# Kernel tuning notes

Hardware: AMD Instinct MI355X
Metric: run time of the kernel (lower is better)

Reference implementation:

```python
import jax, jax.numpy as jnp
import numpy as np
import math

B, T, C = 1, 2048, 2048
H, KVH = 32, 8
D = C // H  # 64
EPS = 1e-5
ROPE_THETA = 10000.0


def rmsnorm(x, w):
    # RMSNorm over last axis (head_dim), matches flax RMSNorm applied per-head
    var = jnp.mean(jnp.square(x), axis=-1, keepdims=True)
    return x * jax.lax.rsqrt(var + EPS) * w


def apply_rope(x, cos, sin):
    # x: [B, T, h, D]; cos/sin: [T, D//2]
    xr = x.reshape(*x.shape[:-1], D // 2, 2)
    x0, x1 = xr[..., 0], xr[..., 1]
    c = cos.reshape(1, T, 1, D // 2)
    s = sin.reshape(1, T, 1, D // 2)
    o0 = x0 * c - x1 * s
    o1 = x0 * s + x1 * c
    return jnp.stack([o0, o1], axis=-1).reshape(x.shape)


def setup_inputs() -> dict:
    key = jax.random.key(0)
    ks = jax.random.split(key, 12)
    x = jax.random.normal(ks[0], (B, T, C), jnp.float32)
    # RoPE tables
    inv_freq = 1.0 / (ROPE_THETA ** (np.arange(0, D, 2, dtype=np.float32) / D))
    angles = np.arange(T, dtype=np.float32)[:, None] * inv_freq[None, :]  # [T, D//2]
    freqs_cos = jnp.asarray(np.cos(angles))
    freqs_sin = jnp.asarray(np.sin(angles))
    # causal additive mask [1,1,T,T]
    causal = np.triu(np.full((T, T), -1e9, dtype=np.float32), k=1)
    mask = jnp.asarray(causal)[None, None]
    sc = lambda f: 1.0 / math.sqrt(f)
    return {
        "x": x,
        "freqs_cos": freqs_cos,
        "freqs_sin": freqs_sin,
        "mask": mask,
        "wq_k": jax.random.normal(ks[1], (C, H * D), jnp.float32) * sc(C),
        "wq_b": jnp.zeros((H * D,), jnp.float32),
        "wk_k": jax.random.normal(ks[2], (C, KVH * D), jnp.float32) * sc(C),
        "wk_b": jnp.zeros((KVH * D,), jnp.float32),
        "wv_k": jax.random.normal(ks[3], (C, KVH * D), jnp.float32) * sc(C),
        "wv_b": jnp.zeros((KVH * D,), jnp.float32),
        "wo_k": jax.random.normal(ks[4], (H * D, C), jnp.float32) * sc(H * D),
        "wo_b": jnp.zeros((C,), jnp.float32),
        "qn_w": jnp.ones((D,), jnp.float32),
        "kn_w": jnp.ones((D,), jnp.float32),
    }


def reference(x, freqs_cos, freqs_sin, mask, wq_k, wq_b, wk_k, wk_b, wv_k, wv_b, wo_k, wo_b, qn_w, kn_w):
    q = (x @ wq_k + wq_b).reshape(B, T, H, D)
    k = (x @ wk_k + wk_b).reshape(B, T, KVH, D)
    v = (x @ wv_k + wv_b).reshape(B, T, KVH, D)
    # QK RMSNorm over head_dim
    q = rmsnorm(q, qn_w)
    k = rmsnorm(k, kn_w)
    # RoPE
    q = apply_rope(q, freqs_cos, freqs_sin)
    k = apply_rope(k, freqs_cos, freqs_sin)
    # GQA repeat kv heads
    rep = H // KVH
    k = jnp.repeat(k, rep, axis=2)
    v = jnp.repeat(v, rep, axis=2)
    # [B, H, T, D]
    q, k, v = (jnp.swapaxes(t, 1, 2) for t in (q, k, v))
    scale = 1.0 / math.sqrt(D)
    scores = jnp.einsum("bhqd,bhkd->bhqk", q, k) * scale + mask
    attn = jax.nn.softmax(scores, axis=-1)
    out = jnp.einsum("bhqk,bhkd->bhqd", attn, v)
    out = jnp.swapaxes(out, 1, 2).reshape(B, T, H * D)
    return out @ wo_k + wo_b
```

## Files before the change

### kernel.cpp

```cpp
#include <hip/hip_runtime.h>
#include <hip/hip_bf16.h>
#include <cstdint>

typedef unsigned short u16;
typedef __attribute__((ext_vector_type(8))) short short8;
typedef __attribute__((ext_vector_type(4))) float f32x4;

__device__ __forceinline__ u16 f2bf(float f) {
  union { float f; uint32_t u; } c; c.f = f;
  return (u16)((c.u + 0x7FFFu + ((c.u >> 16) & 1u)) >> 16);
}

__device__ __forceinline__ uint32_t pack_bf16x2(float a, float b) {
  union { __hip_bfloat162 h; uint32_t u; } c;
  c.h = __float22bfloat162_rn(make_float2(a, b));
  return c.u;
}

__global__ __launch_bounds__(256) void prep_kernel(const float* __restrict__ x,
                                                   u16* __restrict__ xb,
                                                   const float* __restrict__ wq,
                                                   const float* __restrict__ wk,
                                                   const float* __restrict__ wv,
                                                   const float* __restrict__ wo,
                                                   u16* __restrict__ wqkvT,
                                                   u16* __restrict__ woT) {
  int id = blockIdx.x;
  if (id >= 2560) {
    int i = (id - 2560) * 256 + threadIdx.x;
    float4 v = ((const float4*)x)[i];
    ((ushort4*)xb)[i] = make_ushort4(f2bf(v.x), f2bf(v.y), f2bf(v.z), f2bf(v.w));
    return;
  }
  __shared__ float tile[64][65];
  const int K = 2048;
  int bx = id % 80, by = id / 80;
  const float* in; u16* out; int N, nx;
  if (bx < 32)      { in = wq; out = wqkvT;                          N = 2048; nx = bx; }
  else if (bx < 40) { in = wk; out = wqkvT + (size_t)2048 * 2048;    N = 512;  nx = bx - 32; }
  else if (bx < 48) { in = wv; out = wqkvT + (size_t)2560 * 2048;    N = 512;  nx = bx - 40; }
  else              { in = wo; out = woT;                            N = 2048; nx = bx - 48; }
  int n0 = nx * 64, k0 = by * 64;
  int t = threadIdx.x;
  int a = t & 63, b4 = t >> 6;
#pragma unroll
  for (int j = 0; j < 16; ++j) {
    int kk = j * 4 + b4;
    tile[kk][a] = in[(size_t)(k0 + kk) * N + n0 + a];
  }
  __syncthreads();
#pragma unroll
  for (int j = 0; j < 16; ++j) {
    int nn = j * 4 + b4;
    out[(size_t)(n0 + nn) * K + k0 + a] = f2bf(tile[a][nn]);
  }
}

__global__ __launch_bounds__(256, 3) void gemm_qkv(const u16* __restrict__ A,
                                                   const u16* __restrict__ Bt,
                                                   const float* __restrict__ wq_b,
                                                   const float* __restrict__ wk_b,
                                                   const float* __restrict__ wv_b,
                                                   const float* __restrict__ qn_w,
                                                   const float* __restrict__ kn_w,
                                                   const float* __restrict__ fc,
                                                   const float* __restrict__ fs,
                                                   u16* __restrict__ Qg,
                                                   u16* __restrict__ Kg,
                                                   u16* __restrict__ Vgt) {
  const int K = 2048, nb = 24;
  __shared__ alignas(16) u16 As[2][64 * 64];
  __shared__ alignas(16) u16 Bs[2][128 * 64];
  int nwg = gridDim.x;
  int cpx = nwg >> 3;
  int bid = blockIdx.x;
  int swz = (bid & 7) * cpx + (bid >> 3);
  int m0 = (swz / nb) << 6;
  int n0 = (swz % nb) << 7;
  int tid = threadIdx.x;
  int w = tid >> 6, lane = tid & 63;
  int wr = w >> 1, wc = w & 1;
  int fr = lane & 15, hi = lane >> 4;
  int sw = fr & 7;

  auto STAGE = [&](int buf, int kt) {
#pragma unroll
    for (int i = 0; i < 2; ++i) {
      int chunk = i * 256 + tid;
      int row = chunk >> 3, c = chunk & 7;
      const u16* ga = A + (size_t)(m0 + row) * K + kt + ((c ^ (row & 7)) << 3);
      u16* la = &As[buf][(size_t)(i * 256 + w * 64) * 8];
      __builtin_amdgcn_global_load_lds((const __attribute__((address_space(1))) void*)ga,
                                       (__attribute__((address_space(3))) void*)la, 16, 0, 0);
    }
#pragma unroll
    for (int i = 0; i < 4; ++i) {
      int chunk = i * 256 + tid;
      int row = chunk >> 3, c = chunk & 7;
      const u16* gb = Bt + (size_t)(n0 + row) * K + kt + ((c ^ (row & 7)) << 3);
      u16* lb = &Bs[buf][(size_t)(i * 256 + w * 64) * 8];
      __builtin_amdgcn_global_load_lds((const __attribute__((address_space(1))) void*)gb,
                                       (__attribute__((address_space(3))) void*)lb, 16, 0, 0);
    }
  };

  f32x4 acc[2][4] = {};
  STAGE(0, 0);
  __syncthreads();
  int cur = 0;
  int c0 = (hi ^ sw) << 3, c1 = ((4 + hi) ^ sw) << 3;
  for (int kt = 0; kt < K; kt += 64) {
    if (kt + 64 < K) STAGE(cur ^ 1, kt + 64);
    short8 af[2][2], bf[4][2];
#pragma unroll
    for (int m = 0; m < 2; ++m) {
      int rb = (wr * 32 + m * 16 + fr) * 64;
      af[m][0] = *(const short8*)&As[cur][rb + c0];
      af[m][1] = *(const short8*)&As[cur][rb + c1];
    }
#pragma unroll
    for (int n = 0; n < 4; ++n) {
      int rb = (wc * 64 + n * 16 + fr) * 64;
      bf[n][0] = *(const short8*)&Bs[cur][rb + c0];
      bf[n][1] = *(const short8*)&Bs[cur][rb + c1];
    }
#pragma unroll
    for (int m = 0; m < 2; ++m)
#pragma unroll
      for (int n = 0; n < 4; ++n) {
        acc[m][n] = __builtin_amdgcn_mfma_f32_16x16x32_bf16(af[m][0], bf[n][0], acc[m][n], 0, 0, 0);
        acc[m][n] = __builtin_amdgcn_mfma_f32_16x16x32_bf16(af[m][1], bf[n][1], acc[m][n], 0, 0, 0);
      }
    __syncthreads();
    cur ^= 1;
  }

  int fbase = n0 + wc * 64;
  if (fbase >= 2560) {
    const float* bias = wv_b + (fbase - 2560);
    u16* vt = Vgt + (size_t)(fbase - 2560) * 2048;
    float bv[4];
#pragma unroll
    for (int n = 0; n < 4; ++n) bv[n] = bias[n * 16 + fr];
#pragma unroll
    for (int m = 0; m < 2; ++m)
#pragma unroll
      for (int r = 0; r < 4; ++r) {
        int t = m0 + wr * 32 + m * 16 + hi * 4 + r;
#pragma unroll
        for (int n = 0; n < 4; ++n)
          vt[(size_t)(n * 16 + fr) * 2048 + t] = f2bf(acc[m][n][r] + bv[n]);
      }
    return;
  }
  bool isQ = (fbase < 2048);
  const float* bias = isQ ? wq_b + fbase : wk_b + (fbase - 2048);
  const float* nw   = isQ ? qn_w : kn_w;
  float nscale      = isQ ? 0.18033688f : 1.0f;
  u16* outp = isQ ? Qg + (size_t)(fbase >> 6) * 2048 * 64
                  : Kg + (size_t)((fbase - 2048) >> 6) * 2048 * 64;
  float bv[4], nwv[4];
#pragma unroll
  for (int n = 0; n < 4; ++n) {
    bv[n] = bias[n * 16 + fr];
    nwv[n] = nw[n * 16 + fr] * nscale;
  }
#pragma unroll
  for (int m = 0; m < 2; ++m) {
#pragma unroll
    for (int r = 0; r < 4; ++r) {
      int t = m0 + wr * 32 + m * 16 + hi * 4 + r;
      float v[4];
      float sq = 0.0f;
#pragma unroll
      for (int n = 0; n < 4; ++n) { v[n] = acc[m][n][r] + bv[n]; sq += v[n] * v[n]; }
      sq += __shfl_xor(sq, 1); sq += __shfl_xor(sq, 2);
      sq += __shfl_xor(sq, 4); sq += __shfl_xor(sq, 8);
      float rr = rsqrtf(sq * (1.0f / 64.0f) + 1e-5f);
#pragma unroll
      for (int n = 0; n < 4; ++n) {
        float vn = v[n] * rr * nwv[n];
        float part = __shfl_xor(vn, 1);
        int dh = n * 16 + fr;
        float c = fc[t * 32 + (dh >> 1)];
        float s = fs[t * 32 + (dh >> 1)];
        v[n] = (dh & 1) ? (part * s + vn * c) : (vn * c - part * s);
      }
#pragma unroll
      for (int n = 0; n < 4; ++n)
        outp[(size_t)t * 64 + n * 16 + fr] = f2bf(v[n]);
    }
  }
}

__global__ __launch_bounds__(256, 3) void gemm_bt(const u16* __restrict__ A,
                                                  const u16* __restrict__ Bt,
                                                  float* __restrict__ C,
                                                  const float* __restrict__ bias,
                                                  int M, int N, int K) {
  __shared__ alignas(16) u16 As[2][64 * 64];
  __shared__ alignas(16) u16 Bs[2][128 * 64];
  int nb = N >> 7;
  int nwg = gridDim.x;
  int cpx = nwg >> 3;
  int bid = blockIdx.x;
  int swz = (bid & 7) * cpx + (bid >> 3);
  int m0 = (swz / nb) << 6;
  int n0 = (swz % nb) << 7;
  int tid = threadIdx.x;
  int w = tid >> 6, lane = tid & 63;
  int wr = w >> 1, wc = w & 1;
  int fr = lane & 15, hi = lane >> 4;
  int sw = fr & 7;

  auto STAGE = [&](int buf, int kt) {
#pragma unroll
    for (int i = 0; i < 2; ++i) {
      int chunk = i * 256 + tid;
      int row = chunk >> 3, c = chunk & 7;
      const u16* ga = A + (size_t)(m0 + row) * K + kt + ((c ^ (row & 7)) << 3);
      u16* la = &As[buf][(size_t)(i * 256 + w * 64) * 8];
      __builtin_amdgcn_global_load_lds((const __attribute__((address_space(1))) void*)ga,
                                       (__attribute__((address_space(3))) void*)la, 16, 0, 0);
    }
#pragma unroll
    for (int i = 0; i < 4; ++i) {
      int chunk = i * 256 + tid;
      int row = chunk >> 3, c = chunk & 7;
      const u16* gb = Bt + (size_t)(n0 + row) * K + kt + ((c ^ (row & 7)) << 3);
      u16* lb = &Bs[buf][(size_t)(i * 256 + w * 64) * 8];
      __builtin_amdgcn_global_load_lds((const __attribute__((address_space(1))) void*)gb,
                                       (__attribute__((address_space(3))) void*)lb, 16, 0, 0);
    }
  };

  f32x4 acc[2][4] = {};
  STAGE(0, 0);
  __syncthreads();
  int cur = 0;
  int c0 = (hi ^ sw) << 3, c1 = ((4 + hi) ^ sw) << 3;
  for (int kt = 0; kt < K; kt += 64) {
    if (kt + 64 < K) STAGE(cur ^ 1, kt + 64);
    short8 af[2][2], bf[4][2];
#pragma unroll
    for (int m = 0; m < 2; ++m) {
      int rb = (wr * 32 + m * 16 + fr) * 64;
      af[m][0] = *(const short8*)&As[cur][rb + c0];
      af[m][1] = *(const short8*)&As[cur][rb + c1];
    }
#pragma unroll
    for (int n = 0; n < 4; ++n) {
      int rb = (wc * 64 + n * 16 + fr) * 64;
      bf[n][0] = *(const short8*)&Bs[cur][rb + c0];
      bf[n][1] = *(const short8*)&Bs[cur][rb + c1];
    }
#pragma unroll
    for (int m = 0; m < 2; ++m)
#pragma unroll
      for (int n = 0; n < 4; ++n) {
        acc[m][n] = __builtin_amdgcn_mfma_f32_16x16x32_bf16(af[m][0], bf[n][0], acc[m][n], 0, 0, 0);
        acc[m][n] = __builtin_amdgcn_mfma_f32_16x16x32_bf16(af[m][1], bf[n][1], acc[m][n], 0, 0, 0);
      }
    __syncthreads();
    cur ^= 1;
  }
#pragma unroll
  for (int m = 0; m < 2; ++m) {
#pragma unroll
    for (int n = 0; n < 4; ++n) {
      int gcol = n0 + wc * 64 + n * 16 + fr;
      float bvx = bias ? bias[gcol] : 0.0f;
#pragma unroll
      for (int r = 0; r < 4; ++r) {
        int grow = m0 + wr * 32 + m * 16 + hi * 4 + r;
        C[(size_t)grow * N + gcol] = acc[m][n][r] + bvx;
      }
    }
  }
}

__global__ __launch_bounds__(256, 3) void attn_kernel(const u16* __restrict__ Qg,
                                                      const u16* __restrict__ Kg,
                                                      const u16* __restrict__ Vgt,
                                                      const float* __restrict__ qn_w,
                                                      const float* __restrict__ kn_w,
                                                      u16* __restrict__ att) {
  __shared__ alignas(16) u16 Ks[2][64 * 64];
  __shared__ alignas(16) u16 Vs[2][64 * 64];
  __shared__ alignas(16) uint32_t Ps[4][16 * 36];

  int bid = blockIdx.x;
  int grp = bid >> 8, idx = bid & 255;
  int q0 = idx >> 5, h = idx & 31;
  int qt = (grp == 0) ? q0 : (grp == 1) ? 15 - q0 : (grp == 2) ? 16 + q0 : 31 - q0;
  int kvh = h >> 2;

  int tid = threadIdx.x, w = tid >> 6, lane = tid & 63;
  int fr = lane & 15, hi = lane >> 4, fk = hi * 8;

  float ba = fabsf(qn_w[lane]), bb = fabsf(kn_w[lane]);
#pragma unroll
  for (int off = 32; off >= 1; off >>= 1) {
    ba = fmaxf(ba, __shfl_xor(ba, off));
    bb = fmaxf(bb, __shfl_xor(bb, off));
  }
  float mfix = 11.5416222f * ba * bb;

  const u16* qbase = Qg + ((size_t)h * 2048 + qt * 64 + w * 16 + fr) * 64;
  short8 qf0 = *(const short8*)(qbase + fk);
  short8 qf1 = *(const short8*)(qbase + 32 + fk);
  f32x4 o[4] = {};
  float lrow = 0.0f;

  const u16* Kbase = Kg + (size_t)kvh * 2048 * 64;
  const u16* Vtbase = Vgt + (size_t)kvh * 64 * 2048;
  int row0 = tid >> 3, cc = tid & 7;

  auto stage = [&](int buf, int kt) {
#pragma unroll
    for (int i = 0; i < 2; ++i) {
      int row = i * 32 + row0;
      const u16* srcK = Kbase + ((size_t)(kt * 64 + row)) * 64 + ((cc ^ (row & 7)) << 3);
      u16* dstK = &Ks[buf][(size_t)(i * 256 + w * 64) * 8];
      __builtin_amdgcn_global_load_lds((const __attribute__((address_space(1))) void*)srcK,
                                       (__attribute__((address_space(3))) void*)dstK, 16, 0, 0);
      const u16* srcV = Vtbase + (size_t)row * 2048 + kt * 64 + ((cc ^ (row & 7)) << 3);
      u16* dstV = &Vs[buf][(size_t)(i * 256 + w * 64) * 8];
      __builtin_amdgcn_global_load_lds((const __attribute__((address_space(1))) void*)srcV,
                                       (__attribute__((address_space(3))) void*)dstV, 16, 0, 0);
    }
  };

  stage(0, 0);
  __syncthreads();

  uint32_t* Pw = &Ps[w][0];
  int swzr = (fr & 7) << 4;
  int qrow = qt * 64 + w * 16 + fr;

  for (int kt = 0; kt <= qt; ++kt) {
    int buf = kt & 1;
    bool diag = (kt == qt);
    if (!diag) stage(buf ^ 1, kt + 1);
    const char* KsB = (const char*)&Ks[buf][0];
    const char* VsB = (const char*)&Vs[buf][0];
    f32x4 s4[4] = {};
    __builtin_amdgcn_s_setprio(1);
#pragma unroll
    for (int g = 0; g < 4; ++g) {
      int rb = (g * 16 + fr) * 128;
      short8 b0 = *(const short8*)(KsB + ((rb + hi * 16) ^ swzr));
      short8 b1 = *(const short8*)(KsB + ((rb + 64 + hi * 16) ^ swzr));
      s4[g] = __builtin_amdgcn_mfma_f32_16x16x32_bf16(b0, qf0, s4[g], 0, 0, 0);
      s4[g] = __builtin_amdgcn_mfma_f32_16x16x32_bf16(b1, qf1, s4[g], 0, 0, 0);
    }
    __builtin_amdgcn_s_setprio(0);
    if (diag) {
      int kbase = kt * 64 + hi * 4;
#pragma unroll
      for (int g = 0; g < 4; ++g)
#pragma unroll
        for (int r = 0; r < 4; ++r)
          if (kbase + g * 16 + r > qrow) s4[g][r] = -1e30f;
    }
#pragma unroll
    for (int g = 0; g < 4; ++g) {
      float p0 = exp2f(s4[g][0] - mfix);
      float p1 = exp2f(s4[g][1] - mfix);
      float p2 = exp2f(s4[g][2] - mfix);
      float p3 = exp2f(s4[g][3] - mfix);
      lrow += (p0 + p1) + (p2 + p3);
      uint2 pk = make_uint2(pack_bf16x2(p0, p1), pack_bf16x2(p2, p3));
      *(uint2*)&Pw[fr * 36 + g * 8 + hi * 2] = pk;
    }
    asm volatile("s_waitcnt lgkmcnt(0)" ::: "memory");
    short8 pa0 = *(const short8*)&Pw[fr * 36 + hi * 4];
    short8 pa1 = *(const short8*)&Pw[fr * 36 + 16 + hi * 4];
    __builtin_amdgcn_s_setprio(1);
#pragma unroll
    for (int g2 = 0; g2 < 4; ++g2) {
      int rb = (g2 * 16 + fr) * 128;
      short8 vb0 = *(const short8*)(VsB + ((rb + hi * 16) ^ swzr));
      short8 vb1 = *(const short8*)(VsB + ((rb + 64 + hi * 16) ^ swzr));
      o[g2] = __builtin_amdgcn_mfma_f32_16x16x32_bf16(pa0, vb0, o[g2], 0, 0, 0);
      o[g2] = __builtin_amdgcn_mfma_f32_16x16x32_bf16(pa1, vb1, o[g2], 0, 0, 0);
    }
    __builtin_amdgcn_s_setprio(0);
    __syncthreads();
  }
  float rtot = lrow;
  rtot += __shfl_xor(rtot, 16);
  rtot += __shfl_xor(rtot, 32);
#pragma unroll
  for (int r = 0; r < 4; ++r) {
    float li = __shfl(rtot, hi * 4 + r);
    float inv = 1.0f / li;
    size_t rowoff = (size_t)(qt * 64 + w * 16 + hi * 4 + r) * 2048 + h * 64;
#pragma unroll
    for (int g2 = 0; g2 < 4; ++g2)
      att[rowoff + g2 * 16 + fr] = f2bf(o[g2][r] * inv);
  }
}

extern "C" void kernel_launch(void* const* d_in, const int* in_sizes, int n_in,
                              void* d_out, int out_size, void* d_ws, size_t ws_size,
                              hipStream_t stream) {
  const float* x    = (const float*)d_in[0];
  const float* fc   = (const float*)d_in[1];
  const float* fs   = (const float*)d_in[2];
  const float* wq   = (const float*)d_in[4];
  const float* wq_b = (const float*)d_in[5];
  const float* wk   = (const float*)d_in[6];
  const float* wk_b = (const float*)d_in[7];
  const float* wv   = (const float*)d_in[8];
  const float* wv_b = (const float*)d_in[9];
  const float* wo   = (const float*)d_in[10];
  const float* wo_b = (const float*)d_in[11];
  const float* qn   = (const float*)d_in[12];
  const float* kn   = (const float*)d_in[13];
  float* out = (float*)d_out;

  char* ws = (char*)d_ws;
  u16*  xb    = (u16*)(ws);
  u16*  wqkvT = (u16*)(ws + (size_t)(8  << 20));
  u16*  woT   = (u16*)(ws + (size_t)(20 << 20));
  u16*  Qg    = (u16*)(ws + (size_t)(52 << 20));
  u16*  Kg    = (u16*)(ws + (size_t)(60 << 20));
  u16*  Vgt   = (u16*)(ws + (size_t)(62 << 20));
  u16*  att   = (u16*)(ws + (size_t)(64 << 20));

  prep_kernel<<<6656, 256, 0, stream>>>(x, xb, wq, wk, wv, wo, wqkvT, woT);
  gemm_qkv<<<32 * 24, 256, 0, stream>>>(xb, wqkvT, wq_b, wk_b, wv_b, qn, kn, fc, fs, Qg, Kg, Vgt);
  attn_kernel<<<1024, 256, 0, stream>>>(Qg, Kg, Vgt, qn, kn, att);
  gemm_bt<<<32 * 16, 256, 0, stream>>>(att, woT, out, wo_b, 2048, 2048, 2048);
}
```

Before: 134.0 us.

## Process two adjacent query tiles per attention block to reuse K/V tiles

Each attention block now handles two consecutive 64-row query tiles (2p and 2p+1), so each K/V tile staged in shared memory is used for both. This halves the grid to 512 blocks and roughly halves K/V global traffic and staging overhead. Staging changes from direct global-to-LDS loads to register-staged loads written after compute, and launch bounds drop to 2 waves per SIMD for the extra registers. The risks are lower occupancy, fewer blocks to balance the causal triangle, and less latency hiding.

```diff
diff --git a/kernel.cpp b/kernel.cpp
--- a/kernel.cpp
+++ b/kernel.cpp
@@ -279,7 +279,7 @@
   }
 }
 
-__global__ __launch_bounds__(256, 3) void attn_kernel(const u16* __restrict__ Qg,
+__global__ __launch_bounds__(256, 2) void attn_kernel(const u16* __restrict__ Qg,
                                                       const u16* __restrict__ Kg,
                                                       const u16* __restrict__ Vgt,
                                                       const float* __restrict__ qn_w,
@@ -287,12 +287,13 @@
                                                       u16* __restrict__ att) {
   __shared__ alignas(16) u16 Ks[2][64 * 64];
   __shared__ alignas(16) u16 Vs[2][64 * 64];
-  __shared__ alignas(16) uint32_t Ps[4][16 * 36];
+  __shared__ alignas(16) uint32_t Ps[2][4][16 * 36];
 
   int bid = blockIdx.x;
   int grp = bid >> 8, idx = bid & 255;
   int q0 = idx >> 5, h = idx & 31;
-  int qt = (grp == 0) ? q0 : (grp == 1) ? 15 - q0 : (grp == 2) ? 16 + q0 : 31 - q0;
+  int p = (grp == 0) ? q0 : 15 - q0;
+  int qa = 2 * p, qb = 2 * p + 1;
   int kvh = h >> 2;
 
   int tid = threadIdx.x, w = tid >> 6, lane = tid & 63;
@@ -306,99 +307,167 @@
   }
   float mfix = 11.5416222f * ba * bb;
 
-  const u16* qbase = Qg + ((size_t)h * 2048 + qt * 64 + w * 16 + fr) * 64;
-  short8 qf0 = *(const short8*)(qbase + fk);
-  short8 qf1 = *(const short8*)(qbase + 32 + fk);
-  f32x4 o[4] = {};
-  float lrow = 0.0f;
-
+  const u16* qbaseA = Qg + ((size_t)h * 2048 + qa * 64 + w * 16 + fr) * 64;
+  const u16* qbaseB = Qg + ((size_t)h * 2048 + qb * 64 + w * 16 + fr) * 64;
+  short8 qfa0 = *(const short8*)(qbaseA + fk);
+  short8 qfa1 = *(const short8*)(qbaseA + 32 + fk);
+  short8 qfb0 = *(const short8*)(qbaseB + fk);
+  short8 qfb1 = *(const short8*)(qbaseB + 32 + fk);
+  f32x4 oa[4] = {}, ob[4] = {};
+  float lrowa = 0.0f, lrowb = 0.0f;
+
+  int row0 = tid >> 3, cc = tid & 7;
   const u16* Kbase = Kg + (size_t)kvh * 2048 * 64;
   const u16* Vtbase = Vgt + (size_t)kvh * 64 * 2048;
-  int row0 = tid >> 3, cc = tid & 7;
-
-  auto stage = [&](int buf, int kt) {
-#pragma unroll
-    for (int i = 0; i < 2; ++i) {
-      int row = i * 32 + row0;
-      const u16* srcK = Kbase + ((size_t)(kt * 64 + row)) * 64 + ((cc ^ (row & 7)) << 3);
-      u16* dstK = &Ks[buf][(size_t)(i * 256 + w * 64) * 8];
-      __builtin_amdgcn_global_load_lds((const __attribute__((address_space(1))) void*)srcK,
-                                       (__attribute__((address_space(3))) void*)dstK, 16, 0, 0);
-      const u16* srcV = Vtbase + (size_t)row * 2048 + kt * 64 + ((cc ^ (row & 7)) << 3);
-      u16* dstV = &Vs[buf][(size_t)(i * 256 + w * 64) * 8];
-      __builtin_amdgcn_global_load_lds((const __attribute__((address_space(1))) void*)srcV,
-                                       (__attribute__((address_space(3))) void*)dstV, 16, 0, 0);
-    }
+
+  short8 k0r, k1r, v0r, v1r;
+  auto stage_load = [&](int kt2) {
+    const u16* kb = Kbase + (size_t)kt2 * 64 * 64;
+    k0r = *(const short8*)(kb + row0 * 64 + cc * 8);
+    k1r = *(const short8*)(kb + (32 + row0) * 64 + cc * 8);
+    const u16* vb = Vtbase + (size_t)row0 * 2048 + kt2 * 64 + cc * 8;
+    v0r = *(const short8*)vb;
+    v1r = *(const short8*)(vb + 32 * 2048);
   };
-
-  stage(0, 0);
+  auto stage_write = [&](int buf) {
+    char* KsB = (char*)&Ks[buf][0];
+    char* VsB = (char*)&Vs[buf][0];
+    int offA = (row0 * 128 + cc * 16) ^ ((row0 & 7) << 4);
+    int offB = ((32 + row0) * 128 + cc * 16) ^ ((row0 & 7) << 4);
+    *(short8*)(KsB + offA) = k0r;
+    *(short8*)(KsB + offB) = k1r;
+    *(short8*)(VsB + offA) = v0r;
+    *(short8*)(VsB + offB) = v1r;
+  };
+
+  stage_load(0);
+  stage_write(0);
   __syncthreads();
 
-  uint32_t* Pw = &Ps[w][0];
   int swzr = (fr & 7) << 4;
-  int qrow = qt * 64 + w * 16 + fr;
-
-  for (int kt = 0; kt <= qt; ++kt) {
+  int qrowA = qa * 64 + w * 16 + fr;
+  int qrowB = qb * 64 + w * 16 + fr;
+  int nkt = qb + 1;
+
+  for (int kt = 0; kt < nkt; ++kt) {
     int buf = kt & 1;
-    bool diag = (kt == qt);
-    if (!diag) stage(buf ^ 1, kt + 1);
+    bool lastIter = (kt == qb);
+    if (!lastIter) stage_load(kt + 1);
     const char* KsB = (const char*)&Ks[buf][0];
     const char* VsB = (const char*)&Vs[buf][0];
-    f32x4 s4[4] = {};
-    __builtin_amdgcn_s_setprio(1);
-#pragma unroll
-    for (int g = 0; g < 4; ++g) {
-      int rb = (g * 16 + fr) * 128;
-      short8 b0 = *(const short8*)(KsB + ((rb + hi * 16) ^ swzr));
-      short8 b1 = *(const short8*)(KsB + ((rb + 64 + hi * 16) ^ swzr));
-      s4[g] = __builtin_amdgcn_mfma_f32_16x16x32_bf16(b0, qf0, s4[g], 0, 0, 0);
-      s4[g] = __builtin_amdgcn_mfma_f32_16x16x32_bf16(b1, qf1, s4[g], 0, 0, 0);
-    }
-    __builtin_amdgcn_s_setprio(0);
-    if (diag) {
-      int kbase = kt * 64 + hi * 4;
-#pragma unroll
-      for (int g = 0; g < 4; ++g)
-#pragma unroll
-        for (int r = 0; r < 4; ++r)
-          if (kbase + g * 16 + r > qrow) s4[g][r] = -1e30f;
-    }
-#pragma unroll
-    for (int g = 0; g < 4; ++g) {
-      float p0 = exp2f(s4[g][0] - mfix);
-      float p1 = exp2f(s4[g][1] - mfix);
-      float p2 = exp2f(s4[g][2] - mfix);
-      float p3 = exp2f(s4[g][3] - mfix);
-      lrow += (p0 + p1) + (p2 + p3);
-      uint2 pk = make_uint2(pack_bf16x2(p0, p1), pack_bf16x2(p2, p3));
-      *(uint2*)&Pw[fr * 36 + g * 8 + hi * 2] = pk;
-    }
-    asm volatile("s_waitcnt lgkmcnt(0)" ::: "memory");
-    short8 pa0 = *(const short8*)&Pw[fr * 36 + hi * 4];
-    short8 pa1 = *(const short8*)&Pw[fr * 36 + 16 + hi * 4];
-    __builtin_amdgcn_s_setprio(1);
+
+    if (kt <= qa) {
+      f32x4 s4[4] = {};
+      __builtin_amdgcn_s_setprio(1);
+#pragma unroll
+      for (int g = 0; g < 4; ++g) {
+        int rb = (g * 16 + fr) * 128;
+        short8 b0 = *(const short8*)(KsB + ((rb + hi * 16) ^ swzr));
+        short8 b1 = *(const short8*)(KsB + ((rb + 64 + hi * 16) ^ swzr));
+        s4[g] = __builtin_amdgcn_mfma_f32_16x16x32_bf16(b0, qfa0, s4[g], 0, 0, 0);
+        s4[g] = __builtin_amdgcn_mfma_f32_16x16x32_bf16(b1, qfa1, s4[g], 0, 0, 0);
+      }
+      __builtin_amdgcn_s_setprio(0);
+      if (kt == qa) {
+        int kbase = kt * 64 + hi * 4;
+#pragma unroll
+        for (int g = 0; g < 4; ++g)
+#pragma unroll
+          for (int r = 0; r < 4; ++r)
+            if (kbase + g * 16 + r > qrowA) s4[g][r] = -1e30f;
+      }
+      uint32_t* Pw = &Ps[0][w][0];
+#pragma unroll
+      for (int g = 0; g < 4; ++g) {
+        float p0 = exp2f(s4[g][0] - mfix);
+        float p1 = exp2f(s4[g][1] - mfix);
+        float p2 = exp2f(s4[g][2] - mfix);
+        float p3 = exp2f(s4[g][3] - mfix);
+        lrowa += (p0 + p1) + (p2 + p3);
+        uint2 pk = make_uint2(pack_bf16x2(p0, p1), pack_bf16x2(p2, p3));
+        *(uint2*)&Pw[fr * 36 + g * 8 + hi * 2] = pk;
+      }
+      asm volatile("s_waitcnt lgkmcnt(0)" ::: "memory");
+      short8 pa0 = *(const short8*)&Pw[fr * 36 + hi * 4];
+      short8 pa1 = *(const short8*)&Pw[fr * 36 + 16 + hi * 4];
+      __builtin_amdgcn_s_setprio(1);
+#pragma unroll
+      for (int g2 = 0; g2 < 4; ++g2) {
+        int rb = (g2 * 16 + fr) * 128;
+        short8 vb0 = *(const short8*)(VsB + ((rb + hi * 16) ^ swzr));
+        short8 vb1 = *(const short8*)(VsB + ((rb + 64 + hi * 16) ^ swzr));
+        oa[g2] = __builtin_amdgcn_mfma_f32_16x16x32_bf16(pa0, vb0, oa[g2], 0, 0, 0);
+        oa[g2] = __builtin_amdgcn_mfma_f32_16x16x32_bf16(pa1, vb1, oa[g2], 0, 0, 0);
+      }
+      __builtin_amdgcn_s_setprio(0);
+    }
+
+    {
+      f32x4 s4[4] = {};
+      __builtin_amdgcn_s_setprio(1);
+#pragma unroll
+      for (int g = 0; g < 4; ++g) {
+        int rb = (g * 16 + fr) * 128;
+        short8 b0 = *(const short8*)(KsB + ((rb + hi * 16) ^ swzr));
+        short8 b1 = *(const short8*)(KsB + ((rb + 64 + hi * 16) ^ swzr));
+        s4[g] = __builtin_amdgcn_mfma_f32_16x16x32_bf16(b0, qfb0, s4[g], 0, 0, 0);
+        s4[g] = __builtin_amdgcn_mfma_f32_16x16x32_bf16(b1, qfb1, s4[g], 0, 0, 0);
+      }
+      __builtin_amdgcn_s_setprio(0);
+      if (lastIter) {
+        int kbase = kt * 64 + hi * 4;
+#pragma unroll
+        for (int g = 0; g < 4; ++g)
+#pragma unroll
+          for (int r = 0; r < 4; ++r)
+            if (kbase + g * 16 + r > qrowB) s4[g][r] = -1e30f;
+      }
+      uint32_t* Pw = &Ps[1][w][0];
+#pragma unroll
+      for (int g = 0; g < 4; ++g) {
+        float p0 = exp2f(s4[g][0] - mfix);
+        float p1 = exp2f(s4[g][1] - mfix);
+        float p2 = exp2f(s4[g][2] - mfix);
+        float p3 = exp2f(s4[g][3] - mfix);
+        lrowb += (p0 + p1) + (p2 + p3);
+        uint2 pk = make_uint2(pack_bf16x2(p0, p1), pack_bf16x2(p2, p3));
+        *(uint2*)&Pw[fr * 36 + g * 8 + hi * 2] = pk;
+      }
+      asm volatile("s_waitcnt lgkmcnt(0)" ::: "memory");
+      short8 pa0 = *(const short8*)&Pw[fr * 36 + hi * 4];
+      short8 pa1 = *(const short8*)&Pw[fr * 36 + 16 + hi * 4];
+      __builtin_amdgcn_s_setprio(1);
+#pragma unroll
+      for (int g2 = 0; g2 < 4; ++g2) {
+        int rb = (g2 * 16 + fr) * 128;
+        short8 vb0 = *(const short8*)(VsB + ((rb + hi * 16) ^ swzr));
+        short8 vb1 = *(const short8*)(VsB + ((rb + 64 + hi * 16) ^ swzr));
+        ob[g2] = __builtin_amdgcn_mfma_f32_16x16x32_bf16(pa0, vb0, ob[g2], 0, 0, 0);
+        ob[g2] = __builtin_amdgcn_mfma_f32_16x16x32_bf16(pa1, vb1, ob[g2], 0, 0, 0);
+      }
+      __builtin_amdgcn_s_setprio(0);
+    }
+
+    if (!lastIter) stage_write(buf ^ 1);
+    __syncthreads();
+  }
+
+  float rta = lrowa, rtb = lrowb;
+  rta += __shfl_xor(rta, 16); rta += __shfl_xor(rta, 32);
+  rtb += __shfl_xor(rtb, 16); rtb += __shfl_xor(rtb, 32);
+#pragma unroll
+  for (int r = 0; r < 4; ++r) {
+    float lia = __shfl(rta, hi * 4 + r);
+    float lib = __shfl(rtb, hi * 4 + r);
+    float inva = 1.0f / lia;
+    float invb = 1.0f / lib;
+    size_t rowA = (size_t)(qa * 64 + w * 16 + hi * 4 + r) * 2048 + h * 64;
+    size_t rowB = (size_t)(qb * 64 + w * 16 + hi * 4 + r) * 2048 + h * 64;
 #pragma unroll
     for (int g2 = 0; g2 < 4; ++g2) {
-      int rb = (g2 * 16 + fr) * 128;
-      short8 vb0 = *(const short8*)(VsB + ((rb + hi * 16) ^ swzr));
-      short8 vb1 = *(const short8*)(VsB + ((rb + 64 + hi * 16) ^ swzr));
-      o[g2] = __builtin_amdgcn_mfma_f32_16x16x32_bf16(pa0, vb0, o[g2], 0, 0, 0);
-      o[g2] = __builtin_amdgcn_mfma_f32_16x16x32_bf16(pa1, vb1, o[g2], 0, 0, 0);
-    }
-    __builtin_amdgcn_s_setprio(0);
-    __syncthreads();
-  }
-  float rtot = lrow;
-  rtot += __shfl_xor(rtot, 16);
-  rtot += __shfl_xor(rtot, 32);
-#pragma unroll
-  for (int r = 0; r < 4; ++r) {
-    float li = __shfl(rtot, hi * 4 + r);
-    float inv = 1.0f / li;
-    size_t rowoff = (size_t)(qt * 64 + w * 16 + hi * 4 + r) * 2048 + h * 64;
-#pragma unroll
-    for (int g2 = 0; g2 < 4; ++g2)
-      att[rowoff + g2 * 16 + fr] = f2bf(o[g2][r] * inv);
+      att[rowA + g2 * 16 + fr] = f2bf(oa[g2][r] * inva);
+      att[rowB + g2 * 16 + fr] = f2bf(ob[g2][r] * invb);
+    }
   }
 }
 
@@ -431,6 +500,6 @@
 
   prep_kernel<<<6656, 256, 0, stream>>>(x, xb, wq, wk, wv, wo, wqkvT, woT);
   gemm_qkv<<<32 * 24, 256, 0, stream>>>(xb, wqkvT, wq_b, wk_b, wv_b, qn, kn, fc, fs, Qg, Kg, Vgt);
-  attn_kernel<<<1024, 256, 0, stream>>>(Qg, Kg, Vgt, qn, kn, att);
+  attn_kernel<<<512, 256, 0, stream>>>(Qg, Kg, Vgt, qn, kn, att);
   gemm_bt<<<32 * 16, 256, 0, stream>>>(att, woT, out, wo_b, 2048, 2048, 2048);
 }
```

Result: slower. 138.5 us (+3.4%).
